# Kernel tuning notes

Hardware: AMD Instinct MI355X
Metric: run time of the kernel (lower is better)

The kernel has to match this reference:

```python
import jax, jax.numpy as jnp
import numpy as np

N_LAYERS = 2
HID = 128
HEADS = 4
HEAD_DIM = HID // HEADS
INNER = 512
MAXLEN = 50
BS = 2048
N_ITEMS = 50000


def setup_inputs() -> dict:
    key = jax.random.key(0)
    ks = jax.random.split(key, 32)
    s = 0.02
    emb = jax.random.normal(ks[0], (N_ITEMS, HID), jnp.float32) * s
    emb = emb.at[0].set(0.0)  # padding_idx=0
    inp = {
        "input_ids": jax.random.randint(ks[1], (BS, MAXLEN), 0, N_ITEMS),
        "A": jax.random.uniform(ks[2], (BS, MAXLEN, 2 * MAXLEN), jnp.float32),
        "emb": emb,
        "pos_emb": jax.random.normal(ks[3], (MAXLEN, HID), jnp.float32) * s,
        "mixW": jax.random.normal(ks[4], (N_LAYERS, HID, 2 * HID), jnp.float32) * s,
        "mixb": jnp.zeros((N_LAYERS, HID), jnp.float32),
        "Wq": jax.random.normal(ks[5], (N_LAYERS, HID, HID), jnp.float32) * s,
        "bq": jnp.zeros((N_LAYERS, HID), jnp.float32),
        "Wk": jax.random.normal(ks[6], (N_LAYERS, HID, HID), jnp.float32) * s,
        "bk": jnp.zeros((N_LAYERS, HID), jnp.float32),
        "Wv": jax.random.normal(ks[7], (N_LAYERS, HID, HID), jnp.float32) * s,
        "bv": jnp.zeros((N_LAYERS, HID), jnp.float32),
        "Wo": jax.random.normal(ks[8], (N_LAYERS, HID, HID), jnp.float32) * s,
        "bo": jnp.zeros((N_LAYERS, HID), jnp.float32),
        "ln1g": jnp.ones((N_LAYERS, HID), jnp.float32),
        "ln1b": jnp.zeros((N_LAYERS, HID), jnp.float32),
        "W1": jax.random.normal(ks[9], (N_LAYERS, INNER, HID), jnp.float32) * s,
        "b1": jnp.zeros((N_LAYERS, INNER), jnp.float32),
        "W2": jax.random.normal(ks[10], (N_LAYERS, HID, INNER), jnp.float32) * s,
        "b2": jnp.zeros((N_LAYERS, HID), jnp.float32),
        "ln2g": jnp.ones((N_LAYERS, HID), jnp.float32),
        "ln2b": jnp.zeros((N_LAYERS, HID), jnp.float32),
        "attW": jax.random.normal(ks[11], (1, HID), jnp.float32) * s,
        "attb": jnp.full((1,), 0.1, jnp.float32),
        "sessW": jax.random.normal(ks[12], (HID, 2 * HID), jnp.float32) * s,
        "sessb": jnp.zeros((HID,), jnp.float32),
    }
    return inp


def _layer_norm(x, g, b, eps=1e-5):
    m = x.mean(-1, keepdims=True)
    v = ((x - m) ** 2).mean(-1, keepdims=True)
    return (x - m) * jax.lax.rsqrt(v + eps) * g + b


def _forward(input_ids, A, emb, pos_emb, mixW, mixb, Wq, bq, Wk, bk, Wv, bv,
             Wo, bo, ln1g, ln1b, W1, b1, W2, b2, ln2g, ln2b,
             attW, attb, sessW, sessb):
    bs, L = input_ids.shape
    x = emb[input_ids] + pos_emb[None, :L, :]  # [bs, L, H] (dropout = identity in eval)
    for i in range(N_LAYERS):
        # per-sample in/out adjacency aggregation + concat + linear
        x_in = jnp.einsum('blm,bmd->bld', A[:, :, :L], x)
        x_out = jnp.einsum('blm,bmd->bld', A[:, :, L:2 * L], x)
        x = jnp.concatenate([x_in, x_out], -1) @ mixW[i].T + mixb[i]
        # multi-head self-attention (post-LN encoder layer)
        q = (x @ Wq[i].T + bq[i]).reshape(bs, L, HEADS, HEAD_DIM)
        k = (x @ Wk[i].T + bk[i]).reshape(bs, L, HEADS, HEAD_DIM)
        v = (x @ Wv[i].T + bv[i]).reshape(bs, L, HEADS, HEAD_DIM)
        scores = jnp.einsum('blhd,bmhd->bhlm', q, k) / np.sqrt(HEAD_DIM).astype(np.float32)
        p = jax.nn.softmax(scores, axis=-1)
        o = jnp.einsum('bhlm,bmhd->blhd', p, v).reshape(bs, L, HID)
        o = o @ Wo[i].T + bo[i]
        x = _layer_norm(x + o, ln1g[i], ln1b[i])
        ff = jax.nn.relu(x @ W1[i].T + b1[i]) @ W2[i].T + b2[i]
        x = _layer_norm(x + ff, ln2g[i], ln2b[i])
    out_local = x[:, -1, :]                       # [bs, H]
    att = x @ attW.T + attb                       # [bs, L, 1]
    att = att / att.sum(axis=1, keepdims=True)    # sum-normalized attention
    out_glob = jnp.einsum('bld,bl->bd', x, att[..., 0])
    sess = jnp.concatenate([out_local, out_glob], -1) @ sessW.T + sessb  # [bs, H]
    logits = sess @ emb[1:].T                     # tied-embedding GEMM, [bs, n_items-1]
    return logits


def reference(input_ids, A, emb, pos_emb, mixW, mixb, Wq, bq, Wk, bk, Wv, bv,
              Wo, bo, ln1g, ln1b, W1, b1, W2, b2, ln2g, ln2b,
              attW, attb, sessW, sessb):
    return _forward(input_ids, A, emb, pos_emb, mixW, mixb, Wq, bq, Wk, bk, Wv, bv,
                    Wo, bo, ln1g, ln1b, W1, b1, W2, b2, ln2g, ln2b,
                    attW, attb, sessW, sessb)
```

## Files before the change

### kernel.cpp

```cpp
#include <hip/hip_runtime.h>

#define BSZ 2048
#define SEQ 50
#define HID 128
#define NHEAD 4
#define HDIM 32
#define INNER 512
#define NITEMS 50000
#define NOUT 49999
#define NPAD3 51200

typedef float f32x4 __attribute__((ext_vector_type(4)));
typedef short s16x8 __attribute__((ext_vector_type(8)));

__device__ __forceinline__ unsigned short f2b(float f){
  unsigned int u = __builtin_bit_cast(unsigned int, f);
  u = (u + 0x7FFFu + ((u >> 16) & 1u)) >> 16;
  return (unsigned short)u;
}
__device__ __forceinline__ float b2f(unsigned short h){
  unsigned int u = ((unsigned int)h) << 16;
  return __builtin_bit_cast(float, u);
}
__device__ __forceinline__ size_t pk(int n, int k, int ksteps){
  return ((size_t)((n >> 4)*ksteps + (k >> 5))*64 + ((k >> 3) & 3)*16 + (n & 15))*8 + (k & 7);
}

__global__ void embed_k(const int* __restrict__ ids, const float* __restrict__ emb,
                        const float* __restrict__ pos, float* __restrict__ x){
  int row = blockIdx.x;
  int l = row % SEQ;
  int t = threadIdx.x;
  int id = ids[row];
  x[(size_t)row*HID + t] = emb[(size_t)id*HID + t] + pos[l*HID + t];
}

__global__ void cvtw2_k(const float* __restrict__ W1, const float* __restrict__ W2,
                        unsigned short* __restrict__ W1h, unsigned short* __restrict__ W1l,
                        unsigned short* __restrict__ W2h, unsigned short* __restrict__ W2l){
  int i = blockIdx.x*256 + threadIdx.x;
  {
    int l = i >> 16, rc = i & 65535;
    int n = rc >> 7, k = rc & 127;
    float w = W1[i];
    unsigned short h = f2b(w);
    size_t off = (size_t)l*65536 + pk(n, k, 4);
    W1h[off] = h; W1l[off] = f2b(w - b2f(h));
  }
  {
    int l = i >> 16, rc = i & 65535;
    int n = rc >> 9, k = rc & 511;
    float w = W2[i];
    unsigned short h = f2b(w);
    size_t off = (size_t)l*65536 + pk(n, k, 16);
    W2h[off] = h; W2l[off] = f2b(w - b2f(h));
  }
}

__global__ void cvtw_qkvo_k(const float* __restrict__ Wq, const float* __restrict__ Wk,
                            const float* __restrict__ Wv, const float* __restrict__ Wo,
                            unsigned short* __restrict__ dst){
  int i = blockIdx.x*256 + threadIdx.x;
  int l = i >> 14;
  int rc = i & 16383;
  int r = rc >> 7, k = rc & 127;
  unsigned short* Wqkvh = dst;
  unsigned short* Wqkvl = dst + 98304;
  unsigned short* Woh   = dst + 196608;
  unsigned short* Wol   = dst + 229376;
  size_t base = (size_t)l*49152;
  float w; unsigned short h;
  w = Wq[i]; h = f2b(w);
  { size_t o = base + pk(r, k, 4);        Wqkvh[o] = h; Wqkvl[o] = f2b(w - b2f(h)); }
  w = Wk[i]; h = f2b(w);
  { size_t o = base + pk(128 + r, k, 4);  Wqkvh[o] = h; Wqkvl[o] = f2b(w - b2f(h)); }
  w = Wv[i]; h = f2b(w);
  { size_t o = base + pk(256 + r, k, 4);  Wqkvh[o] = h; Wqkvl[o] = f2b(w - b2f(h)); }
  w = Wo[i]; h = f2b(w);
  { size_t o = (size_t)l*16384 + pk(r, k, 4); Woh[o] = h; Wol[o] = f2b(w - b2f(h)); }
}

__global__ void cvtmix_k(const float* __restrict__ mixW,
                         unsigned short* __restrict__ mWh, unsigned short* __restrict__ mWl){
  int i = blockIdx.x*256 + threadIdx.x;
  int l = i >> 15, rc = i & 32767;
  int n = rc >> 8, k = rc & 255;
  float w = mixW[i];
  unsigned short h = f2b(w);
  size_t off = (size_t)l*32768 + pk(n, k, 8);
  mWh[off] = h; mWl[off] = f2b(w - b2f(h));
}

__global__ void cvt_logits_k(const float* __restrict__ sess, const float* __restrict__ emb,
                             unsigned short* __restrict__ sessH, unsigned short* __restrict__ sessL,
                             unsigned short* __restrict__ embH, unsigned short* __restrict__ embL){
  int i = blockIdx.x*256 + threadIdx.x;
  int n = i >> 7, k = i & 127;
  float w = (n < NOUT) ? emb[(size_t)(1+n)*HID + k] : 0.f;
  unsigned short h = f2b(w);
  size_t off = pk(n, k, 4);
  embH[off] = h; embL[off] = f2b(w - b2f(h));
  if (i < BSZ*HID){
    float s = sess[i];
    unsigned short hs = f2b(s);
    sessH[i] = hs; sessL[i] = f2b(s - b2f(hs));
  }
}

__global__ __launch_bounds__(256) void mix_mfma_k(
    const float* __restrict__ A, const float* __restrict__ x,
    const unsigned short* __restrict__ mWh, const unsigned short* __restrict__ mWl,
    const float* __restrict__ mixb, float* __restrict__ xout)
{
  __shared__ __align__(16) char smem[65536];
  char* xTh = smem;
  char* xTl = smem + 16384;
  char* Ah  = smem + 32768;
  char* Al  = smem + 49152;
  char* Ch  = smem;
  char* Cl  = smem + 32768;

  int t = threadIdx.x;
  int wave = t >> 6, lane = t & 63;
  int g = lane >> 4, c16 = lane & 15;
  int b = blockIdx.x;
  size_t xbase = (size_t)b * SEQ * HID;

  {
    s16x8 z = {0,0,0,0,0,0,0,0};
    #pragma unroll
    for (int it = 0; it < 16; ++it)
      *(s16x8*)(smem + (it*256 + t)*16) = z;
  }
  __syncthreads();

  for (int task = t; task < SEQ*32; task += 256){
    int r = task >> 5, c4 = task & 31;
    float4 v = *(const float4*)(x + xbase + (size_t)r*HID + c4*4);
    float f[4] = {v.x, v.y, v.z, v.w};
    #pragma unroll
    for (int i = 0; i < 4; ++i){
      int d = c4*4 + i;
      unsigned short hi = f2b(f[i]);
      unsigned short lo = f2b(f[i] - b2f(hi));
      int off = d*128 + ((((r >> 3) ^ (d & 7))<<4)) + (r & 7)*2;
      *(unsigned short*)(xTh + off) = hi;
      *(unsigned short*)(xTl + off) = lo;
    }
  }
  {
    int l = t >> 2, q = t & 3;
    if (l < SEQ){
      const float* Ar = A + (size_t)(b*SEQ + l)*100;
      for (int j = q*25; j < q*25 + 25; ++j){
        float av = Ar[j];
        int col = (j < SEQ) ? j : (64 + (j - SEQ));
        unsigned short hi = f2b(av);
        unsigned short lo = f2b(av - b2f(hi));
        int off = l*256 + ((((col >> 3) ^ (l & 15))<<4)) + (col & 7)*2;
        *(unsigned short*)(Ah + off) = hi;
        *(unsigned short*)(Al + off) = lo;
      }
    }
  }
  __syncthreads();

  int rA = wave*16 + c16;
  s16x8 aih[2], ail[2], aoh[2], aol[2];
  #pragma unroll
  for (int kt = 0; kt < 2; ++kt){
    int ci = kt*4 + g;
    int co = 8 + kt*4 + g;
    int offi = rA*256 + ((ci ^ (rA & 15))<<4);
    int offo = rA*256 + ((co ^ (rA & 15))<<4);
    aih[kt] = *(const s16x8*)(Ah + offi);
    ail[kt] = *(const s16x8*)(Al + offi);
    aoh[kt] = *(const s16x8*)(Ah + offo);
    aol[kt] = *(const s16x8*)(Al + offo);
  }
  f32x4 accin[8], accout[8];
  #pragma unroll
  for (int nt = 0; nt < 8; ++nt){ accin[nt] = (f32x4){0,0,0,0}; accout[nt] = (f32x4){0,0,0,0}; }
  #pragma unroll
  for (int kt = 0; kt < 2; ++kt){
    #pragma unroll
    for (int nt = 0; nt < 8; ++nt){
      int d = nt*16 + c16;
      int boff = d*128 + ((((kt*4 + g) ^ (d & 7)))<<4);
      s16x8 bh = *(const s16x8*)(xTh + boff);
      s16x8 bl = *(const s16x8*)(xTl + boff);
      accin[nt]  = __builtin_amdgcn_mfma_f32_16x16x32_bf16(aih[kt], bh, accin[nt], 0,0,0);
      accin[nt]  = __builtin_amdgcn_mfma_f32_16x16x32_bf16(aih[kt], bl, accin[nt], 0,0,0);
      accin[nt]  = __builtin_amdgcn_mfma_f32_16x16x32_bf16(ail[kt], bh, accin[nt], 0,0,0);
      accout[nt] = __builtin_amdgcn_mfma_f32_16x16x32_bf16(aoh[kt], bh, accout[nt], 0,0,0);
      accout[nt] = __builtin_amdgcn_mfma_f32_16x16x32_bf16(aoh[kt], bl, accout[nt], 0,0,0);
      accout[nt] = __builtin_amdgcn_mfma_f32_16x16x32_bf16(aol[kt], bh, accout[nt], 0,0,0);
    }
  }
  __syncthreads();

  #pragma unroll
  for (int nt = 0; nt < 8; ++nt){
    #pragma unroll
    for (int r = 0; r < 4; ++r){
      int l = wave*16 + g*4 + r;
      int ci_ = nt*16 + c16;
      float vi = accin[nt][r];
      unsigned short hi = f2b(vi);
      int offi = l*512 + (((ci_ >> 3) ^ (l & 15))<<4) + (ci_ & 7)*2;
      *(unsigned short*)(Ch + offi) = hi;
      *(unsigned short*)(Cl + offi) = f2b(vi - b2f(hi));
      int co_ = 128 + nt*16 + c16;
      float vo = accout[nt][r];
      unsigned short ho = f2b(vo);
      int offo = l*512 + (((co_ >> 3) ^ (l & 15))<<4) + (co_ & 7)*2;
      *(unsigned short*)(Ch + offo) = ho;
      *(unsigned short*)(Cl + offo) = f2b(vo - b2f(ho));
    }
  }
  __syncthreads();

  int rc = wave*16 + c16;
  f32x4 acc2[8];
  #pragma unroll
  for (int nt = 0; nt < 8; ++nt) acc2[nt] = (f32x4){0,0,0,0};
  for (int kt2 = 0; kt2 < 8; ++kt2){
    int slot = (kt2*4 + g) ^ (rc & 15);
    s16x8 cfh = *(const s16x8*)(Ch + rc*512 + slot*16);
    s16x8 cfl = *(const s16x8*)(Cl + rc*512 + slot*16);
    #pragma unroll
    for (int nt = 0; nt < 8; ++nt){
      s16x8 wh = *(const s16x8*)(mWh + (size_t)(nt*8 + kt2)*512 + lane*8);
      s16x8 wl = *(const s16x8*)(mWl + (size_t)(nt*8 + kt2)*512 + lane*8);
      acc2[nt] = __builtin_amdgcn_mfma_f32_16x16x32_bf16(cfh, wh, acc2[nt], 0,0,0);
      acc2[nt] = __builtin_amdgcn_mfma_f32_16x16x32_bf16(cfh, wl, acc2[nt], 0,0,0);
      acc2[nt] = __builtin_amdgcn_mfma_f32_16x16x32_bf16(cfl, wh, acc2[nt], 0,0,0);
    }
  }
  #pragma unroll
  for (int nt = 0; nt < 8; ++nt){
    int j = nt*16 + c16;
    float bb = mixb[j];
    #pragma unroll
    for (int r = 0; r < 4; ++r){
      int l = wave*16 + g*4 + r;
      if (l < SEQ) xout[xbase + (size_t)l*HID + j] = acc2[nt][r] + bb;
    }
  }
}

__global__ __launch_bounds__(256) void qkv_mfma_k(
    const float* __restrict__ x,
    const unsigned short* __restrict__ Wh, const unsigned short* __restrict__ Wl,
    const float* __restrict__ bq, const float* __restrict__ bk,
    const float* __restrict__ bv, float* __restrict__ qkv)
{
  __shared__ unsigned short Xh[64*128];
  __shared__ unsigned short Xl[64*128];
  int t = threadIdx.x;
  int wave = t >> 6, lane = t & 63;
  int g = lane >> 4, c16 = lane & 15;
  int wrh = wave >> 1;
  int wn  = wave & 1;
  size_t row0 = (size_t)blockIdx.x * 64;

  #pragma unroll
  for (int it = 0; it < 4; ++it){
    int idx8 = it*256 + t;
    int r = idx8 >> 4;
    int c8 = idx8 & 15;
    const float* src = x + (row0 + r)*HID + c8*8;
    float4 v0 = *(const float4*)(src);
    float4 v1 = *(const float4*)(src + 4);
    float f[8] = {v0.x,v0.y,v0.z,v0.w,v1.x,v1.y,v1.z,v1.w};
    s16x8 ph, pl;
    #pragma unroll
    for (int e = 0; e < 8; ++e){
      unsigned short hi = f2b(f[e]);
      ph[e] = (short)hi;
      pl[e] = (short)f2b(f[e] - b2f(hi));
    }
    int slot = c8 ^ (r & 15);
    *(s16x8*)((char*)Xh + r*256 + slot*16) = ph;
    *(s16x8*)((char*)Xl + r*256 + slot*16) = pl;
  }
  __syncthreads();

  int rl0 = wrh*16 + c16;
  int rl1 = 32 + rl0;
  s16x8 a0h[4], a0l[4], a1h[4], a1l[4];
  #pragma unroll
  for (int kt = 0; kt < 4; ++kt){
    int slot = (kt*4 + g) ^ (rl0 & 15);
    a0h[kt] = *(const s16x8*)((const char*)Xh + rl0*256 + slot*16);
    a0l[kt] = *(const s16x8*)((const char*)Xl + rl0*256 + slot*16);
    a1h[kt] = *(const s16x8*)((const char*)Xh + rl1*256 + slot*16);
    a1l[kt] = *(const s16x8*)((const char*)Xl + rl1*256 + slot*16);
  }

  for (int nt = 0; nt < 12; ++nt){
    int tile = wn*12 + nt;
    int ncol = tile*16 + c16;
    f32x4 acc0 = {0.f,0.f,0.f,0.f};
    f32x4 acc1 = {0.f,0.f,0.f,0.f};
    #pragma unroll
    for (int kt = 0; kt < 4; ++kt){
      s16x8 bh = *(const s16x8*)(Wh + (size_t)(tile*4 + kt)*512 + lane*8);
      s16x8 bl = *(const s16x8*)(Wl + (size_t)(tile*4 + kt)*512 + lane*8);
      acc0 = __builtin_amdgcn_mfma_f32_16x16x32_bf16(a0h[kt], bh, acc0, 0,0,0);
      acc0 = __builtin_amdgcn_mfma_f32_16x16x32_bf16(a0h[kt], bl, acc0, 0,0,0);
      acc0 = __builtin_amdgcn_mfma_f32_16x16x32_bf16(a0l[kt], bh, acc0, 0,0,0);
      acc1 = __builtin_amdgcn_mfma_f32_16x16x32_bf16(a1h[kt], bh, acc1, 0,0,0);
      acc1 = __builtin_amdgcn_mfma_f32_16x16x32_bf16(a1h[kt], bl, acc1, 0,0,0);
      acc1 = __builtin_amdgcn_mfma_f32_16x16x32_bf16(a1l[kt], bh, acc1, 0,0,0);
    }
    int mat = ncol >> 7;
    int colin = ncol & 127;
    float bias = (mat == 0) ? bq[colin] : (mat == 1 ? bk[colin] : bv[colin]);
    #pragma unroll
    for (int r = 0; r < 4; ++r){
      int m = wrh*16 + g*4 + r;
      qkv[(row0 + m)*384 + ncol] = acc0[r] + bias;
      qkv[(row0 + 32 + m)*384 + ncol] = acc1[r] + bias;
    }
  }
}

__global__ void attn_core_k(const float* __restrict__ qkv, float* __restrict__ o){
  int blk = blockIdx.x; int b = blk / NHEAD; int h = blk % NHEAD;
  int t = threadIdx.x;
  __shared__ float qs[SEQ][HDIM];
  __shared__ float ks[SEQ][HDIM];
  __shared__ float vs[SEQ][HDIM];
  __shared__ float ss[SEQ][SEQ+2];
  size_t base = (size_t)b*SEQ*384 + h*HDIM;
  for (int task = t; task < SEQ*HDIM; task += 256){
    int l = task >> 5, d = task & 31;
    const float* p = qkv + base + (size_t)l*384 + d;
    qs[l][d] = p[0];
    ks[l][d] = p[128];
    vs[l][d] = p[256];
  }
  __syncthreads();
  for (int task = t; task < SEQ*SEQ; task += 256){
    int l = task / SEQ, m = task % SEQ;
    float a = 0.f;
    #pragma unroll
    for (int d = 0; d < HDIM; ++d) a += qs[l][d]*ks[m][d];
    ss[l][m] = a * 0.17677669529663687f;
  }
  __syncthreads();
  if (t < SEQ){
    float mx = -1e30f;
    for (int m = 0; m < SEQ; ++m) mx = fmaxf(mx, ss[t][m]);
    float sum = 0.f;
    for (int m = 0; m < SEQ; ++m){ float e = __expf(ss[t][m]-mx); ss[t][m]=e; sum+=e; }
    float inv = 1.f/sum;
    for (int m = 0; m < SEQ; ++m) ss[t][m] *= inv;
  }
  __syncthreads();
  for (int task = t; task < SEQ*HDIM; task += 256){
    int l = task >> 5, d = task & 31;
    float a = 0.f;
    for (int m = 0; m < SEQ; ++m) a += ss[l][m]*vs[m][d];
    o[((size_t)b*SEQ+l)*HID + h*HDIM + d] = a;
  }
}

__global__ __launch_bounds__(256) void oproj_mfma_k(
    const float* __restrict__ o,
    const unsigned short* __restrict__ Woh_, const unsigned short* __restrict__ Wol_,
    const float* __restrict__ bo, const float* __restrict__ g1,
    const float* __restrict__ be1, float* x)
{
  __shared__ unsigned short Oh[64*128];
  __shared__ unsigned short Ol[64*128];
  __shared__ float red_s[2][2][2][16];
  __shared__ float red_q[2][2][2][16];
  int t = threadIdx.x;
  int wave = t >> 6, lane = t & 63;
  int g = lane >> 4, c16 = lane & 15;
  int wrh = wave >> 1;
  int wn  = wave & 1;
  size_t row0 = (size_t)blockIdx.x * 64;

  #pragma unroll
  for (int it = 0; it < 4; ++it){
    int idx8 = it*256 + t;
    int r = idx8 >> 4;
    int c8 = idx8 & 15;
    const float* src = o + (row0 + r)*HID + c8*8;
    float4 v0 = *(const float4*)(src);
    float4 v1 = *(const float4*)(src + 4);
    float f[8] = {v0.x,v0.y,v0.z,v0.w,v1.x,v1.y,v1.z,v1.w};
    s16x8 ph, pl;
    #pragma unroll
    for (int e = 0; e < 8; ++e){
      unsigned short hi = f2b(f[e]);
      ph[e] = (short)hi;
      pl[e] = (short)f2b(f[e] - b2f(hi));
    }
    int slot = c8 ^ (r & 15);
    *(s16x8*)((char*)Oh + r*256 + slot*16) = ph;
    *(s16x8*)((char*)Ol + r*256 + slot*16) = pl;
  }
  __syncthreads();

  int rl0 = wrh*16 + c16;
  int rl1 = 32 + rl0;
  s16x8 a0h[4], a0l[4], a1h[4], a1l[4];
  #pragma unroll
  for (int kt = 0; kt < 4; ++kt){
    int slot = (kt*4 + g) ^ (rl0 & 15);
    a0h[kt] = *(const s16x8*)((const char*)Oh + rl0*256 + slot*16);
    a0l[kt] = *(const s16x8*)((const char*)Ol + rl0*256 + slot*16);
    a1h[kt] = *(const s16x8*)((const char*)Oh + rl1*256 + slot*16);
    a1l[kt] = *(const s16x8*)((const char*)Ol + rl1*256 + slot*16);
  }

  float vals[2][4][4];
  #pragma unroll
  for (int nt = 0; nt < 4; ++nt){
    int tile = wn*4 + nt;
    int jcol = tile*16 + c16;
    f32x4 acc0 = {0.f,0.f,0.f,0.f};
    f32x4 acc1 = {0.f,0.f,0.f,0.f};
    #pragma unroll
    for (int kt = 0; kt < 4; ++kt){
      s16x8 bh = *(const s16x8*)(Woh_ + (size_t)(tile*4 + kt)*512 + lane*8);
      s16x8 bl = *(const s16x8*)(Wol_ + (size_t)(tile*4 + kt)*512 + lane*8);
      acc0 = __builtin_amdgcn_mfma_f32_16x16x32_bf16(a0h[kt], bh, acc0, 0,0,0);
      acc0 = __builtin_amdgcn_mfma_f32_16x16x32_bf16(a0h[kt], bl, acc0, 0,0,0);
      acc0 = __builtin_amdgcn_mfma_f32_16x16x32_bf16(a0l[kt], bh, acc0, 0,0,0);
      acc1 = __builtin_amdgcn_mfma_f32_16x16x32_bf16(a1h[kt], bh, acc1, 0,0,0);
      acc1 = __builtin_amdgcn_mfma_f32_16x16x32_bf16(a1h[kt], bl, acc1, 0,0,0);
      acc1 = __builtin_amdgcn_mfma_f32_16x16x32_bf16(a1l[kt], bh, acc1, 0,0,0);
    }
    float bias = bo[jcol];
    #pragma unroll
    for (int r = 0; r < 4; ++r){
      int m = wrh*16 + g*4 + r;
      vals[0][nt][r] = acc0[r] + bias + x[(row0 + m)*HID + jcol];
      vals[1][nt][r] = acc1[r] + bias + x[(row0 + 32 + m)*HID + jcol];
    }
  }

  #pragma unroll
  for (int q_ = 0; q_ < 2; ++q_){
    #pragma unroll
    for (int r = 0; r < 4; ++r){
      float s_ = vals[q_][0][r] + vals[q_][1][r] + vals[q_][2][r] + vals[q_][3][r];
      float qq = vals[q_][0][r]*vals[q_][0][r] + vals[q_][1][r]*vals[q_][1][r]
               + vals[q_][2][r]*vals[q_][2][r] + vals[q_][3][r]*vals[q_][3][r];
      s_ += __shfl_xor(s_, 1, 64); qq += __shfl_xor(qq, 1, 64);
      s_ += __shfl_xor(s_, 2, 64); qq += __shfl_xor(qq, 2, 64);
      s_ += __shfl_xor(s_, 4, 64); qq += __shfl_xor(qq, 4, 64);
      s_ += __shfl_xor(s_, 8, 64); qq += __shfl_xor(qq, 8, 64);
      if (c16 == 0){
        red_s[q_][wrh][wn][g*4 + r] = s_;
        red_q[q_][wrh][wn][g*4 + r] = qq;
      }
    }
  }
  __syncthreads();
  #pragma unroll
  for (int q_ = 0; q_ < 2; ++q_){
    #pragma unroll
    for (int r = 0; r < 4; ++r){
      int m = wrh*16 + g*4 + r;
      float s_tot = red_s[q_][wrh][0][g*4 + r] + red_s[q_][wrh][1][g*4 + r];
      float q_tot = red_q[q_][wrh][0][g*4 + r] + red_q[q_][wrh][1][g*4 + r];
      float mean = s_tot * (1.f/HID);
      float var = q_tot * (1.f/HID) - mean*mean;
      float rstd = rsqrtf(var + 1e-5f);
      #pragma unroll
      for (int nt = 0; nt < 4; ++nt){
        int jcol = (wn*4 + nt)*16 + c16;
        x[(row0 + q_*32 + m)*HID + jcol] = (vals[q_][nt][r]-mean)*rstd*g1[jcol] + be1[jcol];
      }
    }
  }
}

__global__ __launch_bounds__(256) void ffn1_k(
    const float* __restrict__ x,
    const unsigned short* __restrict__ W1h, const unsigned short* __restrict__ W1l,
    const float* __restrict__ b1,
    unsigned short* __restrict__ Hph, unsigned short* __restrict__ Hpl)
{
  __shared__ unsigned short Xh[64*128];
  __shared__ unsigned short Xl[64*128];
  int t = threadIdx.x;
  int wave = t >> 6, lane = t & 63;
  int g = lane >> 4, c16 = lane & 15;
  int wrh = wave >> 1;
  int wn  = wave & 1;
  size_t row0 = (size_t)blockIdx.x * 64;

  #pragma unroll
  for (int it = 0; it < 4; ++it){
    int idx8 = it*256 + t;
    int r = idx8 >> 4;
    int c8 = idx8 & 15;
    const float* src = x + (row0 + r)*HID + c8*8;
    float4 v0 = *(const float4*)(src);
    float4 v1 = *(const float4*)(src + 4);
    float f[8] = {v0.x,v0.y,v0.z,v0.w,v1.x,v1.y,v1.z,v1.w};
    s16x8 ph, pl;
    #pragma unroll
    for (int e = 0; e < 8; ++e){
      unsigned short hi = f2b(f[e]);
      ph[e] = (short)hi;
      pl[e] = (short)f2b(f[e] - b2f(hi));
    }
    int slot = c8 ^ (r & 15);
    *(s16x8*)((char*)Xh + r*256 + slot*16) = ph;
    *(s16x8*)((char*)Xl + r*256 + slot*16) = pl;
  }
  __syncthreads();

  int rl0 = wrh*16 + c16;
  int rl1 = 32 + rl0;
  s16x8 a0h[4], a0l[4], a1h[4], a1l[4];
  #pragma unroll
  for (int kt = 0; kt < 4; ++kt){
    int slot = (kt*4 + g) ^ (rl0 & 15);
    a0h[kt] = *(const s16x8*)((const char*)Xh + rl0*256 + slot*16);
    a0l[kt] = *(const s16x8*)((const char*)Xl + rl0*256 + slot*16);
    a1h[kt] = *(const s16x8*)((const char*)Xh + rl1*256 + slot*16);
    a1l[kt] = *(const s16x8*)((const char*)Xl + rl1*256 + slot*16);
  }

  for (int nt = 0; nt < 16; ++nt){
    int tile = wn*16 + nt;
    int ncol = tile*16 + c16;
    f32x4 acc0 = {0.f,0.f,0.f,0.f};
    f32x4 acc1 = {0.f,0.f,0.f,0.f};
    #pragma unroll
    for (int kt = 0; kt < 4; ++kt){
      s16x8 bh = *(const s16x8*)(W1h + (size_t)(tile*4 + kt)*512 + lane*8);
      s16x8 bl = *(const s16x8*)(W1l + (size_t)(tile*4 + kt)*512 + lane*8);
      acc0 = __builtin_amdgcn_mfma_f32_16x16x32_bf16(a0h[kt], bh, acc0, 0,0,0);
      acc0 = __builtin_amdgcn_mfma_f32_16x16x32_bf16(a0h[kt], bl, acc0, 0,0,0);
      acc0 = __builtin_amdgcn_mfma_f32_16x16x32_bf16(a0l[kt], bh, acc0, 0,0,0);
      acc1 = __builtin_amdgcn_mfma_f32_16x16x32_bf16(a1h[kt], bh, acc1, 0,0,0);
      acc1 = __builtin_amdgcn_mfma_f32_16x16x32_bf16(a1h[kt], bl, acc1, 0,0,0);
      acc1 = __builtin_amdgcn_mfma_f32_16x16x32_bf16(a1l[kt], bh, acc1, 0,0,0);
    }
    float bias = b1[ncol];
    #pragma unroll
    for (int r = 0; r < 4; ++r){
      int m0 = (int)row0 + wrh*16 + g*4 + r;
      float h0 = fmaxf(acc0[r] + bias, 0.f);
      unsigned short hh0 = f2b(h0);
      size_t o0 = pk(m0, ncol, 16);
      Hph[o0] = hh0; Hpl[o0] = f2b(h0 - b2f(hh0));
      float h1 = fmaxf(acc1[r] + bias, 0.f);
      unsigned short hh1 = f2b(h1);
      size_t o1 = pk(m0 + 32, ncol, 16);
      Hph[o1] = hh1; Hpl[o1] = f2b(h1 - b2f(hh1));
    }
  }
}

__global__ __launch_bounds__(256) void ffn2_k(
    const unsigned short* __restrict__ Hph, const unsigned short* __restrict__ Hpl,
    const unsigned short* __restrict__ W2h, const unsigned short* __restrict__ W2l,
    const float* __restrict__ b2, const float* __restrict__ gam,
    const float* __restrict__ bet, float* x)
{
  __shared__ float red_s[2][2][16];
  __shared__ float red_q[2][2][16];
  int t = threadIdx.x;
  int wave = t >> 6, lane = t & 63;
  int g = lane >> 4, c16 = lane & 15;
  int wrh = wave >> 1;
  int wn  = wave & 1;
  size_t row0 = (size_t)blockIdx.x * 32;
  int rt = (int)(row0 >> 4) + wrh;

  f32x4 acc2[4];
  #pragma unroll
  for (int i = 0; i < 4; ++i) acc2[i] = (f32x4){0.f,0.f,0.f,0.f};
  for (int kt2 = 0; kt2 < 16; ++kt2){
    s16x8 hfh = *(const s16x8*)(Hph + (size_t)(rt*16 + kt2)*512 + lane*8);
    s16x8 hfl = *(const s16x8*)(Hpl + (size_t)(rt*16 + kt2)*512 + lane*8);
    #pragma unroll
    for (int nt2 = 0; nt2 < 4; ++nt2){
      int tile = wn*4 + nt2;
      s16x8 wfh = *(const s16x8*)(W2h + (size_t)(tile*16 + kt2)*512 + lane*8);
      s16x8 wfl = *(const s16x8*)(W2l + (size_t)(tile*16 + kt2)*512 + lane*8);
      acc2[nt2] = __builtin_amdgcn_mfma_f32_16x16x32_bf16(wfh, hfh, acc2[nt2], 0,0,0);
      acc2[nt2] = __builtin_amdgcn_mfma_f32_16x16x32_bf16(wfh, hfl, acc2[nt2], 0,0,0);
      acc2[nt2] = __builtin_amdgcn_mfma_f32_16x16x32_bf16(wfl, hfh, acc2[nt2], 0,0,0);
    }
  }

  int hrow = wrh*16 + c16;
  size_t grow = row0 + (size_t)hrow;
  const float* xr = x + grow*HID;
  float vals[16];
  float s = 0.f, q = 0.f;
  #pragma unroll
  for (int nt2 = 0; nt2 < 4; ++nt2){
    #pragma unroll
    for (int r = 0; r < 4; ++r){
      int j = (wn*4 + nt2)*16 + g*4 + r;
      float v = acc2[nt2][r] + b2[j] + xr[j];
      vals[nt2*4+r] = v;
      s += v; q += v*v;
    }
  }
  s += __shfl_xor(s, 16, 64);
  s += __shfl_xor(s, 32, 64);
  q += __shfl_xor(q, 16, 64);
  q += __shfl_xor(q, 32, 64);
  if (g == 0){
    red_s[wrh][wn][c16] = s;
    red_q[wrh][wn][c16] = q;
  }
  __syncthreads();
  float s_tot = red_s[wrh][0][c16] + red_s[wrh][1][c16];
  float q_tot = red_q[wrh][0][c16] + red_q[wrh][1][c16];
  float mean = s_tot * (1.f/HID);
  float var = q_tot * (1.f/HID) - mean*mean;
  float rstd = rsqrtf(var + 1e-5f);
  float* orow = x + grow*HID;
  #pragma unroll
  for (int nt2 = 0; nt2 < 4; ++nt2){
    #pragma unroll
    for (int r = 0; r < 4; ++r){
      int j = (wn*4 + nt2)*16 + g*4 + r;
      orow[j] = (vals[nt2*4+r]-mean)*rstd*gam[j] + bet[j];
    }
  }
}

__global__ void final_k(const float* __restrict__ x, const float* __restrict__ attW,
                        const float* __restrict__ attb, const float* __restrict__ sessW,
                        const float* __restrict__ sessb, float* __restrict__ sess){
  int b = blockIdx.x; int t = threadIdx.x;
  __shared__ float av[SEQ];
  __shared__ __align__(16) float cat[256];
  const float* xb = x + (size_t)b*SEQ*HID;
  if (t < SEQ){
    float a = attb[0];
    for (int c = 0; c < HID; ++c) a += xb[t*HID + c]*attW[c];
    av[t] = a;
  }
  __syncthreads();
  if (t == 0){
    float s = 0.f;
    for (int l = 0; l < SEQ; ++l) s += av[l];
    float inv = 1.f/s;
    for (int l = 0; l < SEQ; ++l) av[l] *= inv;
  }
  __syncthreads();
  float gacc = 0.f;
  for (int l = 0; l < SEQ; ++l) gacc += xb[l*HID + t]*av[l];
  cat[t] = xb[49*HID + t];
  cat[128+t] = gacc;
  __syncthreads();
  float acc = sessb[t];
  const float4* w = (const float4*)(sessW + (size_t)t*256);
  const float4* c4 = (const float4*)cat;
  #pragma unroll 8
  for (int j = 0; j < 64; ++j){
    float4 wv=w[j]; float4 cv=c4[j];
    acc += wv.x*cv.x + wv.y*cv.y + wv.z*cv.z + wv.w*cv.w;
  }
  sess[(size_t)b*HID + t] = acc;
}

__global__ __launch_bounds__(256) void logits_mfma_k(
    const unsigned short* __restrict__ sessH, const unsigned short* __restrict__ sessL,
    const unsigned short* __restrict__ embH, const unsigned short* __restrict__ embL,
    float* __restrict__ out)
{
  __shared__ unsigned short Sh[32*128];
  __shared__ unsigned short Sl[32*128];
  __shared__ float Ob[32*132];
  int t = threadIdx.x;
  int wave = t >> 6, lane = t & 63;
  int g = lane >> 4, c16 = lane & 15;
  int wrh = wave >> 1;
  int wn  = wave & 1;
  int id = blockIdx.x;
  int xcd = id & 7;
  int j = id >> 3;
  int dslab = xcd*25 + (j >> 6);
  int rowt = j & 63;
  size_t row0 = (size_t)rowt * 32;

  #pragma unroll
  for (int it = 0; it < 2; ++it){
    int idx8 = it*256 + t;
    int r = idx8 >> 4;
    int c8 = idx8 & 15;
    s16x8 ph = *(const s16x8*)(sessH + (row0 + r)*HID + c8*8);
    s16x8 pl = *(const s16x8*)(sessL + (row0 + r)*HID + c8*8);
    int slot = c8 ^ (r & 15);
    *(s16x8*)((char*)Sh + r*256 + slot*16) = ph;
    *(s16x8*)((char*)Sl + r*256 + slot*16) = pl;
  }
  __syncthreads();

  int rloc = wrh*16 + c16;
  s16x8 afh[4], afl[4];
  #pragma unroll
  for (int kt = 0; kt < 4; ++kt){
    int slot = (kt*4 + g) ^ (rloc & 15);
    afh[kt] = *(const s16x8*)((const char*)Sh + rloc*256 + slot*16);
    afl[kt] = *(const s16x8*)((const char*)Sl + rloc*256 + slot*16);
  }

  #pragma unroll
  for (int ph = 0; ph < 2; ++ph){
    int n0 = dslab*256 + ph*128;
    #pragma unroll
    for (int nt = 0; nt < 4; ++nt){
      int tb = (n0 >> 4) + wn*4 + nt;
      int ncol = n0 + (wn*4 + nt)*16 + c16;
      f32x4 acc = {0.f,0.f,0.f,0.f};
      #pragma unroll
      for (int kt = 0; kt < 4; ++kt){
        s16x8 bh = *(const s16x8*)(embH + (size_t)(tb*4 + kt)*512 + lane*8);
        s16x8 bl = *(const s16x8*)(embL + (size_t)(tb*4 + kt)*512 + lane*8);
        acc = __builtin_amdgcn_mfma_f32_16x16x32_bf16(afh[kt], bh, acc, 0,0,0);
        acc = __builtin_amdgcn_mfma_f32_16x16x32_bf16(afh[kt], bl, acc, 0,0,0);
        acc = __builtin_amdgcn_mfma_f32_16x16x32_bf16(afl[kt], bh, acc, 0,0,0);
      }
      #pragma unroll
      for (int r = 0; r < 4; ++r){
        int m = wrh*16 + g*4 + r;
        Ob[m*132 + (wn*4 + nt)*16 + c16] = acc[r];
      }
    }
    __syncthreads();

    #pragma unroll
    for (int k = 0; k < 16; ++k){
      int idx = k*256 + t;
      int r_ = idx >> 7;
      int c_ = idx & 127;
      int ncol = n0 + c_;
      if (ncol < NOUT){
        __builtin_nontemporal_store(Ob[r_*132 + c_],
                                    out + (row0 + r_)*(size_t)NOUT + ncol);
      }
    }
    __syncthreads();
  }
}

extern "C" void kernel_launch(void* const* d_in, const int* in_sizes, int n_in,
                              void* d_out, int out_size, void* d_ws, size_t ws_size,
                              hipStream_t stream){
  const int*   ids  = (const int*)d_in[0];
  const float* A    = (const float*)d_in[1];
  const float* emb  = (const float*)d_in[2];
  const float* pos  = (const float*)d_in[3];
  const float* mixW = (const float*)d_in[4];
  const float* mixb = (const float*)d_in[5];
  const float* Wq   = (const float*)d_in[6];
  const float* bq   = (const float*)d_in[7];
  const float* Wk   = (const float*)d_in[8];
  const float* bk   = (const float*)d_in[9];
  const float* Wv   = (const float*)d_in[10];
  const float* bv   = (const float*)d_in[11];
  const float* Wo   = (const float*)d_in[12];
  const float* bo   = (const float*)d_in[13];
  const float* ln1g = (const float*)d_in[14];
  const float* ln1b = (const float*)d_in[15];
  const float* W1   = (const float*)d_in[16];
  const float* b1   = (const float*)d_in[17];
  const float* W2   = (const float*)d_in[18];
  const float* b2   = (const float*)d_in[19];
  const float* ln2g = (const float*)d_in[20];
  const float* ln2b = (const float*)d_in[21];
  const float* attW = (const float*)d_in[22];
  const float* attb = (const float*)d_in[23];
  const float* sessW= (const float*)d_in[24];
  const float* sessb= (const float*)d_in[25];
  float* out = (float*)d_out;

  float* xA   = (float*)d_ws;
  float* xB   = xA + (size_t)BSZ*SEQ*HID;
  float* sess = xB + (size_t)BSZ*SEQ*HID;
  unsigned short* W1h = (unsigned short*)sess;
  unsigned short* W1l = W1h + (size_t)2*INNER*HID;
  unsigned short* W2h = W1l + (size_t)2*INNER*HID;
  unsigned short* W2l = W2h + (size_t)2*INNER*HID;
  unsigned short* awb = (unsigned short*)(out + (size_t)out_size - 131072);
  unsigned short* Wqkvh = awb;
  unsigned short* Wqkvl = awb + 98304;
  unsigned short* Woh   = awb + 196608;
  unsigned short* Wol   = awb + 229376;
  unsigned short* mwb = (unsigned short*)(out + (size_t)out_size - 131072 - 65536);
  unsigned short* mWh = mwb;
  unsigned short* mWl = mwb + 65536;
  float* qkvbuf = out;
  float* obuf   = out + (size_t)102400*384;
  unsigned short* Hph = (unsigned short*)out;
  unsigned short* Hpl = Hph + (size_t)102400*INNER;
  unsigned short* embHs = (unsigned short*)xB;
  unsigned short* embLs = embHs + (size_t)NPAD3*HID;
  unsigned short* sessH = embLs + (size_t)NPAD3*HID;
  unsigned short* sessL = sessH + (size_t)BSZ*HID;

  cvtw2_k<<<512, 256, 0, stream>>>(W1, W2, W1h, W1l, W2h, W2l);
  cvtw_qkvo_k<<<128, 256, 0, stream>>>(Wq, Wk, Wv, Wo, awb);
  cvtmix_k<<<256, 256, 0, stream>>>(mixW, mWh, mWl);
  embed_k<<<BSZ*SEQ, HID, 0, stream>>>(ids, emb, pos, xA);
  float* xc = xA; float* xn = xB;
  for (int i = 0; i < 2; ++i){
    mix_mfma_k<<<BSZ, 256, 0, stream>>>(A, xc,
        mWh + (size_t)i*HID*256, mWl + (size_t)i*HID*256, mixb + i*HID, xn);
    qkv_mfma_k<<<BSZ*SEQ/64, 256, 0, stream>>>(xn,
        Wqkvh + (size_t)i*384*HID, Wqkvl + (size_t)i*384*HID,
        bq + i*HID, bk + i*HID, bv + i*HID, qkvbuf);
    attn_core_k<<<BSZ*NHEAD, 256, 0, stream>>>(qkvbuf, obuf);
    oproj_mfma_k<<<BSZ*SEQ/64, 256, 0, stream>>>(obuf,
        Woh + (size_t)i*HID*HID, Wol + (size_t)i*HID*HID,
        bo + i*HID, ln1g + i*HID, ln1b + i*HID, xn);
    ffn1_k<<<BSZ*SEQ/64, 256, 0, stream>>>(xn,
        W1h + (size_t)i*INNER*HID, W1l + (size_t)i*INNER*HID, b1 + i*INNER,
        Hph, Hpl);
    ffn2_k<<<BSZ*SEQ/32, 256, 0, stream>>>(Hph, Hpl,
        W2h + (size_t)i*INNER*HID, W2l + (size_t)i*INNER*HID, b2 + i*HID,
        ln2g + i*HID, ln2b + i*HID, xn);
    float* tmp = xc; xc = xn; xn = tmp;
  }
  final_k<<<BSZ, HID, 0, stream>>>(xc, attW, attb, sessW, sessb, sess);
  cvt_logits_k<<<NPAD3*HID/256, 256, 0, stream>>>(sess, emb, sessH, sessL, embHs, embLs);
  logits_mfma_k<<<8*25*64, 256, 0, stream>>>(sessH, sessL, embHs, embLs, out);
}
```

Measured before the change: 1.524 ms.

## Emit pre-split bf16 MFMA-packed activations from producer kernels

Producer kernels (mix, attention core, out-projection+LN) now write their outputs directly as hi/lo bf16 pairs in the MFMA fragment-packed layout. The consumer GEMM kernels (qkv, oproj, ffn1) load A-fragments straight from global memory and no longer stage through shared memory or do conversion. This removes the per-consumer fp32 read, split-conversion and LDS round trip plus a barrier. In exchange it adds scattered 2-byte global stores in the producers and reorganises scratch buffer aliasing inside the output buffer.

```diff
diff --git a/kernel.cpp b/kernel.cpp
--- a/kernel.cpp
+++ b/kernel.cpp
@@ -9,6 +9,7 @@
 #define NITEMS 50000
 #define NOUT 49999
 #define NPAD3 51200
+#define NROWS (BSZ*SEQ)
 
 typedef float f32x4 __attribute__((ext_vector_type(4)));
 typedef short s16x8 __attribute__((ext_vector_type(8)));
@@ -110,7 +111,8 @@
 __global__ __launch_bounds__(256) void mix_mfma_k(
     const float* __restrict__ A, const float* __restrict__ x,
     const unsigned short* __restrict__ mWh, const unsigned short* __restrict__ mWl,
-    const float* __restrict__ mixb, float* __restrict__ xout)
+    const float* __restrict__ mixb, float* __restrict__ xout,
+    unsigned short* __restrict__ xPh, unsigned short* __restrict__ xPl)
 {
   __shared__ __align__(16) char smem[65536];
   char* xTh = smem;
@@ -244,58 +246,39 @@
     #pragma unroll
     for (int r = 0; r < 4; ++r){
       int l = wave*16 + g*4 + r;
-      if (l < SEQ) xout[xbase + (size_t)l*HID + j] = acc2[nt][r] + bb;
+      if (l < SEQ){
+        float v = acc2[nt][r] + bb;
+        xout[xbase + (size_t)l*HID + j] = v;
+        int gr = b*SEQ + l;
+        unsigned short hh = f2b(v);
+        size_t po = pk(gr, j, 4);
+        xPh[po] = hh; xPl[po] = f2b(v - b2f(hh));
+      }
     }
   }
 }
 
 __global__ __launch_bounds__(256) void qkv_mfma_k(
-    const float* __restrict__ x,
+    const unsigned short* __restrict__ xPh, const unsigned short* __restrict__ xPl,
     const unsigned short* __restrict__ Wh, const unsigned short* __restrict__ Wl,
     const float* __restrict__ bq, const float* __restrict__ bk,
     const float* __restrict__ bv, float* __restrict__ qkv)
 {
-  __shared__ unsigned short Xh[64*128];
-  __shared__ unsigned short Xl[64*128];
   int t = threadIdx.x;
   int wave = t >> 6, lane = t & 63;
   int g = lane >> 4, c16 = lane & 15;
   int wrh = wave >> 1;
   int wn  = wave & 1;
   size_t row0 = (size_t)blockIdx.x * 64;
-
-  #pragma unroll
-  for (int it = 0; it < 4; ++it){
-    int idx8 = it*256 + t;
-    int r = idx8 >> 4;
-    int c8 = idx8 & 15;
-    const float* src = x + (row0 + r)*HID + c8*8;
-    float4 v0 = *(const float4*)(src);
-    float4 v1 = *(const float4*)(src + 4);
-    float f[8] = {v0.x,v0.y,v0.z,v0.w,v1.x,v1.y,v1.z,v1.w};
-    s16x8 ph, pl;
-    #pragma unroll
-    for (int e = 0; e < 8; ++e){
-      unsigned short hi = f2b(f[e]);
-      ph[e] = (short)hi;
-      pl[e] = (short)f2b(f[e] - b2f(hi));
-    }
-    int slot = c8 ^ (r & 15);
-    *(s16x8*)((char*)Xh + r*256 + slot*16) = ph;
-    *(s16x8*)((char*)Xl + r*256 + slot*16) = pl;
-  }
-  __syncthreads();
-
-  int rl0 = wrh*16 + c16;
-  int rl1 = 32 + rl0;
+  int rt0 = (int)(row0 >> 4) + wrh;
+
   s16x8 a0h[4], a0l[4], a1h[4], a1l[4];
   #pragma unroll
   for (int kt = 0; kt < 4; ++kt){
-    int slot = (kt*4 + g) ^ (rl0 & 15);
-    a0h[kt] = *(const s16x8*)((const char*)Xh + rl0*256 + slot*16);
-    a0l[kt] = *(const s16x8*)((const char*)Xl + rl0*256 + slot*16);
-    a1h[kt] = *(const s16x8*)((const char*)Xh + rl1*256 + slot*16);
-    a1l[kt] = *(const s16x8*)((const char*)Xl + rl1*256 + slot*16);
+    a0h[kt] = *(const s16x8*)(xPh + (size_t)(rt0*4 + kt)*512 + lane*8);
+    a0l[kt] = *(const s16x8*)(xPl + (size_t)(rt0*4 + kt)*512 + lane*8);
+    a1h[kt] = *(const s16x8*)(xPh + (size_t)((rt0+2)*4 + kt)*512 + lane*8);
+    a1l[kt] = *(const s16x8*)(xPl + (size_t)((rt0+2)*4 + kt)*512 + lane*8);
   }
 
   for (int nt = 0; nt < 12; ++nt){
@@ -326,7 +309,9 @@
   }
 }
 
-__global__ void attn_core_k(const float* __restrict__ qkv, float* __restrict__ o){
+__global__ void attn_core_k(const float* __restrict__ qkv,
+                            unsigned short* __restrict__ oPh,
+                            unsigned short* __restrict__ oPl){
   int blk = blockIdx.x; int b = blk / NHEAD; int h = blk % NHEAD;
   int t = threadIdx.x;
   __shared__ float qs[SEQ][HDIM];
@@ -363,18 +348,21 @@
     int l = task >> 5, d = task & 31;
     float a = 0.f;
     for (int m = 0; m < SEQ; ++m) a += ss[l][m]*vs[m][d];
-    o[((size_t)b*SEQ+l)*HID + h*HDIM + d] = a;
+    int gr = b*SEQ + l;
+    int k = h*HDIM + d;
+    unsigned short hh = f2b(a);
+    size_t po = pk(gr, k, 4);
+    oPh[po] = hh; oPl[po] = f2b(a - b2f(hh));
   }
 }
 
 __global__ __launch_bounds__(256) void oproj_mfma_k(
-    const float* __restrict__ o,
+    const unsigned short* __restrict__ oPh, const unsigned short* __restrict__ oPl,
     const unsigned short* __restrict__ Woh_, const unsigned short* __restrict__ Wol_,
     const float* __restrict__ bo, const float* __restrict__ g1,
-    const float* __restrict__ be1, float* x)
+    const float* __restrict__ be1, float* x,
+    unsigned short* __restrict__ xQh, unsigned short* __restrict__ xQl)
 {
-  __shared__ unsigned short Oh[64*128];
-  __shared__ unsigned short Ol[64*128];
   __shared__ float red_s[2][2][2][16];
   __shared__ float red_q[2][2][2][16];
   int t = threadIdx.x;
@@ -383,39 +371,15 @@
   int wrh = wave >> 1;
   int wn  = wave & 1;
   size_t row0 = (size_t)blockIdx.x * 64;
-
-  #pragma unroll
-  for (int it = 0; it < 4; ++it){
-    int idx8 = it*256 + t;
-    int r = idx8 >> 4;
-    int c8 = idx8 & 15;
-    const float* src = o + (row0 + r)*HID + c8*8;
-    float4 v0 = *(const float4*)(src);
-    float4 v1 = *(const float4*)(src + 4);
-    float f[8] = {v0.x,v0.y,v0.z,v0.w,v1.x,v1.y,v1.z,v1.w};
-    s16x8 ph, pl;
-    #pragma unroll
-    for (int e = 0; e < 8; ++e){
-      unsigned short hi = f2b(f[e]);
-      ph[e] = (short)hi;
-      pl[e] = (short)f2b(f[e] - b2f(hi));
-    }
-    int slot = c8 ^ (r & 15);
-    *(s16x8*)((char*)Oh + r*256 + slot*16) = ph;
-    *(s16x8*)((char*)Ol + r*256 + slot*16) = pl;
-  }
-  __syncthreads();
-
-  int rl0 = wrh*16 + c16;
-  int rl1 = 32 + rl0;
+  int rt0 = (int)(row0 >> 4) + wrh;
+
   s16x8 a0h[4], a0l[4], a1h[4], a1l[4];
   #pragma unroll
   for (int kt = 0; kt < 4; ++kt){
-    int slot = (kt*4 + g) ^ (rl0 & 15);
-    a0h[kt] = *(const s16x8*)((const char*)Oh + rl0*256 + slot*16);
-    a0l[kt] = *(const s16x8*)((const char*)Ol + rl0*256 + slot*16);
-    a1h[kt] = *(const s16x8*)((const char*)Oh + rl1*256 + slot*16);
-    a1l[kt] = *(const s16x8*)((const char*)Ol + rl1*256 + slot*16);
+    a0h[kt] = *(const s16x8*)(oPh + (size_t)(rt0*4 + kt)*512 + lane*8);
+    a0l[kt] = *(const s16x8*)(oPl + (size_t)(rt0*4 + kt)*512 + lane*8);
+    a1h[kt] = *(const s16x8*)(oPh + (size_t)((rt0+2)*4 + kt)*512 + lane*8);
+    a1l[kt] = *(const s16x8*)(oPl + (size_t)((rt0+2)*4 + kt)*512 + lane*8);
   }
 
   float vals[2][4][4];
@@ -476,59 +440,38 @@
       #pragma unroll
       for (int nt = 0; nt < 4; ++nt){
         int jcol = (wn*4 + nt)*16 + c16;
-        x[(row0 + q_*32 + m)*HID + jcol] = (vals[q_][nt][r]-mean)*rstd*g1[jcol] + be1[jcol];
+        int grow = (int)row0 + q_*32 + m;
+        float v = (vals[q_][nt][r]-mean)*rstd*g1[jcol] + be1[jcol];
+        x[(size_t)grow*HID + jcol] = v;
+        unsigned short hh = f2b(v);
+        size_t po = pk(grow, jcol, 4);
+        xQh[po] = hh; xQl[po] = f2b(v - b2f(hh));
       }
     }
   }
 }
 
 __global__ __launch_bounds__(256) void ffn1_k(
-    const float* __restrict__ x,
+    const unsigned short* __restrict__ xQh, const unsigned short* __restrict__ xQl,
     const unsigned short* __restrict__ W1h, const unsigned short* __restrict__ W1l,
     const float* __restrict__ b1,
     unsigned short* __restrict__ Hph, unsigned short* __restrict__ Hpl)
 {
-  __shared__ unsigned short Xh[64*128];
-  __shared__ unsigned short Xl[64*128];
   int t = threadIdx.x;
   int wave = t >> 6, lane = t & 63;
   int g = lane >> 4, c16 = lane & 15;
   int wrh = wave >> 1;
   int wn  = wave & 1;
   size_t row0 = (size_t)blockIdx.x * 64;
-
-  #pragma unroll
-  for (int it = 0; it < 4; ++it){
-    int idx8 = it*256 + t;
-    int r = idx8 >> 4;
-    int c8 = idx8 & 15;
-    const float* src = x + (row0 + r)*HID + c8*8;
-    float4 v0 = *(const float4*)(src);
-    float4 v1 = *(const float4*)(src + 4);
-    float f[8] = {v0.x,v0.y,v0.z,v0.w,v1.x,v1.y,v1.z,v1.w};
-    s16x8 ph, pl;
-    #pragma unroll
-    for (int e = 0; e < 8; ++e){
-      unsigned short hi = f2b(f[e]);
-      ph[e] = (short)hi;
-      pl[e] = (short)f2b(f[e] - b2f(hi));
-    }
-    int slot = c8 ^ (r & 15);
-    *(s16x8*)((char*)Xh + r*256 + slot*16) = ph;
-    *(s16x8*)((char*)Xl + r*256 + slot*16) = pl;
-  }
-  __syncthreads();
-
-  int rl0 = wrh*16 + c16;
-  int rl1 = 32 + rl0;
+  int rt0 = (int)(row0 >> 4) + wrh;
+
   s16x8 a0h[4], a0l[4], a1h[4], a1l[4];
   #pragma unroll
   for (int kt = 0; kt < 4; ++kt){
-    int slot = (kt*4 + g) ^ (rl0 & 15);
-    a0h[kt] = *(const s16x8*)((const char*)Xh + rl0*256 + slot*16);
-    a0l[kt] = *(const s16x8*)((const char*)Xl + rl0*256 + slot*16);
-    a1h[kt] = *(const s16x8*)((const char*)Xh + rl1*256 + slot*16);
-    a1l[kt] = *(const s16x8*)((const char*)Xl + rl1*256 + slot*16);
+    a0h[kt] = *(const s16x8*)(xQh + (size_t)(rt0*4 + kt)*512 + lane*8);
+    a0l[kt] = *(const s16x8*)(xQl + (size_t)(rt0*4 + kt)*512 + lane*8);
+    a1h[kt] = *(const s16x8*)(xQh + (size_t)((rt0+2)*4 + kt)*512 + lane*8);
+    a1l[kt] = *(const s16x8*)(xQl + (size_t)((rt0+2)*4 + kt)*512 + lane*8);
   }
 
   for (int nt = 0; nt < 16; ++nt){
@@ -785,8 +728,8 @@
   float* out = (float*)d_out;
 
   float* xA   = (float*)d_ws;
-  float* xB   = xA + (size_t)BSZ*SEQ*HID;
-  float* sess = xB + (size_t)BSZ*SEQ*HID;
+  float* xB   = xA + (size_t)NROWS*HID;
+  float* sess = xB + (size_t)NROWS*HID;
   unsigned short* W1h = (unsigned short*)sess;
   unsigned short* W1l = W1h + (size_t)2*INNER*HID;
   unsigned short* W2h = W1l + (size_t)2*INNER*HID;
@@ -800,9 +743,14 @@
   unsigned short* mWh = mwb;
   unsigned short* mWl = mwb + 65536;
   float* qkvbuf = out;
-  float* obuf   = out + (size_t)102400*384;
-  unsigned short* Hph = (unsigned short*)out;
-  unsigned short* Hpl = Hph + (size_t)102400*INNER;
+  unsigned short* xPh = (unsigned short*)(out + (size_t)NROWS*384);
+  unsigned short* xPl = xPh + (size_t)NROWS*HID;
+  unsigned short* oPh = xPh;
+  unsigned short* oPl = xPl;
+  unsigned short* xQh = (unsigned short*)out;
+  unsigned short* xQl = xQh + (size_t)NROWS*HID;
+  unsigned short* Hph = (unsigned short*)out + (size_t)2*NROWS*HID;
+  unsigned short* Hpl = Hph + (size_t)NROWS*INNER;
   unsigned short* embHs = (unsigned short*)xB;
   unsigned short* embLs = embHs + (size_t)NPAD3*HID;
   unsigned short* sessH = embLs + (size_t)NPAD3*HID;
@@ -811,22 +759,23 @@
   cvtw2_k<<<512, 256, 0, stream>>>(W1, W2, W1h, W1l, W2h, W2l);
   cvtw_qkvo_k<<<128, 256, 0, stream>>>(Wq, Wk, Wv, Wo, awb);
   cvtmix_k<<<256, 256, 0, stream>>>(mixW, mWh, mWl);
-  embed_k<<<BSZ*SEQ, HID, 0, stream>>>(ids, emb, pos, xA);
+  embed_k<<<NROWS, HID, 0, stream>>>(ids, emb, pos, xA);
   float* xc = xA; float* xn = xB;
   for (int i = 0; i < 2; ++i){
     mix_mfma_k<<<BSZ, 256, 0, stream>>>(A, xc,
-        mWh + (size_t)i*HID*256, mWl + (size_t)i*HID*256, mixb + i*HID, xn);
-    qkv_mfma_k<<<BSZ*SEQ/64, 256, 0, stream>>>(xn,
+        mWh + (size_t)i*HID*256, mWl + (size_t)i*HID*256, mixb + i*HID, xn,
+        xPh, xPl);
+    qkv_mfma_k<<<NROWS/64, 256, 0, stream>>>(xPh, xPl,
         Wqkvh + (size_t)i*384*HID, Wqkvl + (size_t)i*384*HID,
         bq + i*HID, bk + i*HID, bv + i*HID, qkvbuf);
-    attn_core_k<<<BSZ*NHEAD, 256, 0, stream>>>(qkvbuf, obuf);
-    oproj_mfma_k<<<BSZ*SEQ/64, 256, 0, stream>>>(obuf,
+    attn_core_k<<<BSZ*NHEAD, 256, 0, stream>>>(qkvbuf, oPh, oPl);
+    oproj_mfma_k<<<NROWS/64, 256, 0, stream>>>(oPh, oPl,
         Woh + (size_t)i*HID*HID, Wol + (size_t)i*HID*HID,
-        bo + i*HID, ln1g + i*HID, ln1b + i*HID, xn);
-    ffn1_k<<<BSZ*SEQ/64, 256, 0, stream>>>(xn,
+        bo + i*HID, ln1g + i*HID, ln1b + i*HID, xn, xQh, xQl);
+    ffn1_k<<<NROWS/64, 256, 0, stream>>>(xQh, xQl,
         W1h + (size_t)i*INNER*HID, W1l + (size_t)i*INNER*HID, b1 + i*INNER,
         Hph, Hpl);
-    ffn2_k<<<BSZ*SEQ/32, 256, 0, stream>>>(Hph, Hpl,
+    ffn2_k<<<NROWS/32, 256, 0, stream>>>(Hph, Hpl,
         W2h + (size_t)i*INNER*HID, W2l + (size_t)i*INNER*HID, b2 + i*HID,
         ln2g + i*HID, ln2b + i*HID, xn);
     float* tmp = xc; xc = xn; xn = tmp;
```

After: 1.704 ms. 11.8% more time.
